# Optimization experiments

Measured on AMD Instinct MI355X. Metric: run time of the kernel, lower is better.

The kernel has to match this reference:

```python
import jax, jax.numpy as jnp
import numpy as np

EPS = 1e-15
B, N_PER, D, K, DEG = 64, 1024, 256, 64, 16  # graphs, nodes/graph, feat dim, pools/graph, avg degree


def setup_inputs() -> dict:
    key = jax.random.key(0)
    k1, k2, k3, k4 = jax.random.split(key, 4)
    N = B * N_PER
    E = B * N_PER * DEG
    x = jax.random.normal(k1, (N, D), jnp.float32)
    # edges confined within each graph (block-diagonal batched adjacency)
    rng = np.random.default_rng(0)
    offs = np.repeat(np.arange(B, dtype=np.int64) * N_PER, N_PER * DEG)
    src = rng.integers(0, N_PER, size=E) + offs
    dst = rng.integers(0, N_PER, size=E) + offs
    edge_index = jnp.asarray(np.stack([src, dst], axis=0), dtype=jnp.int32)
    edge_weight = jax.random.uniform(k2, (E,), jnp.float32)
    batch_ptr = jnp.arange(B + 1, dtype=jnp.int32) * N_PER
    W = jax.random.normal(k3, (D, K), jnp.float32) * 0.05  # pooling_net = Linear(D, K)
    b = jnp.zeros((K,), jnp.float32)
    gumbel_noise = jax.random.gumbel(k4, (N, K), jnp.float32)
    return {"x": x, "edge_weight": edge_weight, "W": W, "b": b,
            "gumbel_noise": gumbel_noise, "edge_index": edge_index, "batch_ptr": batch_ptr}


def _stochpool(x, edge_weight, W, b, gumbel_noise, edge_index, batch_ptr):
    N, Dd = x.shape
    nb = batch_ptr.shape[0] - 1          # num graphs
    n = N // nb                          # nodes per graph (equal-sized graphs)
    E = edge_index.shape[1]
    e_per = E // nb                      # edges per graph

    # pooling net + hard gumbel softmax (straight-through, tau=1)
    logits = x @ W + b                   # (N, K)
    y_soft = jax.nn.softmax(logits + gumbel_noise, axis=-1)
    y_hard = jax.nn.one_hot(jnp.argmax(y_soft, axis=-1), W.shape[1], dtype=y_soft.dtype)
    s = jax.lax.stop_gradient(y_hard - y_soft) + y_soft   # (N, K)

    u, v = edge_index[0], edge_index[1]
    graph_of_edge = u // n               # (E,) graph id per edge

    s_b = s.reshape(nb, n, -1)           # (B, n, K)
    x_b = x.reshape(nb, n, Dd)

    # pooled features: s^T x per graph
    out = jnp.einsum('bnk,bnd->bkd', s_b, x_b).reshape(nb * s_b.shape[2], Dd)

    # pooled adjacency: s^T A s per graph, via As = scatter-add over edges
    As = jnp.zeros_like(s).at[u].add(edge_weight[:, None] * s[v])   # (N, K) : (A s)
    out_adj = jnp.einsum('bnk,bnl->bkl', s_b, As.reshape(nb, n, -1))  # (B, K, K)

    # link loss: ||A - S S^T||_F per graph, via Frobenius expansion (no n x n dense)
    sq_A = jax.ops.segment_sum(edge_weight * edge_weight, graph_of_edge, num_segments=nb)
    cross = jax.ops.segment_sum(edge_weight * jnp.sum(s[u] * s[v], axis=-1),
                                graph_of_edge, num_segments=nb)
    StS = jnp.einsum('bnk,bnl->bkl', s_b, s_b)                # (B, K, K)
    sq_SSt = jnp.sum(StS * StS, axis=(1, 2))                  # ||S S^T||_F^2 = ||S^T S||_F^2
    link = jnp.sqrt(jnp.maximum(sq_A - 2.0 * cross + sq_SSt, 0.0))
    link = link / e_per                                       # normalize=True
    link_loss = jnp.mean(link)

    entropy_loss = jnp.mean(jnp.sum(-s * jnp.log(s + EPS), axis=-1))

    Kp = s_b.shape[2]
    batch = jnp.repeat(jnp.arange(nb, dtype=jnp.int32), Kp)
    batch_ptr_out = jnp.arange(0, (nb + 1) * Kp, Kp, dtype=jnp.int32)
    return out, out_adj, link_loss, entropy_loss, batch, batch_ptr_out


def reference(x, edge_weight, W, b, gumbel_noise, edge_index, batch_ptr):
    return _stochpool(x, edge_weight, W, b, gumbel_noise, edge_index, batch_ptr)
```

## Files before the change

kernel.cpp:

```cpp
#include <hip/hip_runtime.h>

#define NN 65536
#define DD 256
#define KK 64
#define NPG 1024

#define OUT_OFF   0
#define ADJ_OFF   1048576
#define LINK_OFF  1310720
#define ENT_OFF   1310721
#define BATCH_OFF 1310722
#define BPTR_OFF  1314818

#define WS_S1A    0
#define WS_C      524288
#define WS_SQP    540672
#define WS_CRP    541696
#define WS_ENTP   542720
#define WS_SORTP  552960
#define WS_GOFF   1077248
#define WS_ADJP   1093888
#define WS_NEED   (WS_ADJP + 256 * 4096 * 4)

typedef __bf16 bf16x8 __attribute__((ext_vector_type(8)));
typedef unsigned short u16x8 __attribute__((ext_vector_type(8)));
typedef float f32x4 __attribute__((ext_vector_type(4)));

static __device__ __forceinline__ unsigned short f2bf(float f) {
  unsigned int u = __float_as_uint(f);
  return (unsigned short)((u + 0x7fffu + ((u >> 16) & 1u)) >> 16);
}

__global__ __launch_bounds__(256, 4) void pool_assign_kernel(
    const float* __restrict__ x, const float* __restrict__ Wm,
    const float* __restrict__ bvec, const float* __restrict__ gum,
    int2* __restrict__ s1a, float* __restrict__ entp)
{
  __shared__ unsigned short lds_wt[64 * 264];
  __shared__ float esum[4];
  const int t    = threadIdx.x;
  const int lane = t & 63;
  const int wv   = t >> 6;
  const int q    = lane >> 4;
  const int c    = lane & 15;
  const int nb0  = blockIdx.x << 6;

  #pragma unroll 8
  for (int i = 0; i < 64; ++i) {
    int idx = (i << 8) + t;
    lds_wt[(idx & 63) * 264 + (idx >> 6)] = f2bf(Wm[idx]);
  }

  const int arow = nb0 + (wv << 4) + c;
  const float* xrow = x + (size_t)arow * DD + (q << 3);
  u16x8 afr[8];
  #pragma unroll
  for (int kb = 0; kb < 8; ++kb) {
    float4 u0 = *(const float4*)(xrow + kb * 32);
    float4 u1 = *(const float4*)(xrow + kb * 32 + 4);
    u16x8 af;
    af[0] = f2bf(u0.x); af[1] = f2bf(u0.y); af[2] = f2bf(u0.z); af[3] = f2bf(u0.w);
    af[4] = f2bf(u1.x); af[5] = f2bf(u1.y); af[6] = f2bf(u1.z); af[7] = f2bf(u1.w);
    afr[kb] = af;
  }
  __syncthreads();

  f32x4 acc[4];
  #pragma unroll
  for (int n = 0; n < 4; ++n) acc[n] = (f32x4){0.f, 0.f, 0.f, 0.f};
  #pragma unroll
  for (int n = 0; n < 4; ++n) {
    #pragma unroll
    for (int kb = 0; kb < 8; ++kb) {
      u16x8 bu = *(const u16x8*)(&lds_wt[(n * 16 + c) * 264 + kb * 32 + (q << 3)]);
      acc[n] = __builtin_amdgcn_mfma_f32_16x16x32_bf16(
          __builtin_bit_cast(bf16x8, afr[kb]),
          __builtin_bit_cast(bf16x8, bu), acc[n], 0, 0, 0);
    }
  }

  float bb[4];
  #pragma unroll
  for (int n = 0; n < 4; ++n) bb[n] = bvec[n * 16 + c];
  const int nodeq = nb0 + (wv << 4) + (q << 2);
  float ent = 0.f;
  #pragma unroll
  for (int reg = 0; reg < 4; ++reg) {
    float zz[4];
    #pragma unroll
    for (int n = 0; n < 4; ++n)
      zz[n] = acc[n][reg] + bb[n] + gum[(size_t)(nodeq + reg) * KK + n * 16 + c];
    float m = zz[0]; int a = c;
    #pragma unroll
    for (int n = 1; n < 4; ++n)
      if (zz[n] > m) { m = zz[n]; a = n * 16 + c; }
    #pragma unroll
    for (int mask = 1; mask <= 8; mask <<= 1) {
      float mo = __shfl_xor(m, mask, 64);
      int   ao = __shfl_xor(a, mask, 64);
      if (mo > m || (mo == m && ao < a)) { m = mo; a = ao; }
    }
    float ls = 0.f;
    #pragma unroll
    for (int n = 0; n < 4; ++n) ls += expf(zz[n] - m);
    #pragma unroll
    for (int mask = 1; mask <= 8; mask <<= 1) ls += __shfl_xor(ls, mask, 64);
    if (c == 0) {
      int node = nodeq + reg;
      float p  = 1.0f / ls;
      float s1 = (1.0f - p) + p;
      s1a[node] = make_int2(a, __float_as_int(s1));
      ent += -s1 * logf(s1 + 1e-15f);
    }
  }
  #pragma unroll
  for (int off = 32; off; off >>= 1) ent += __shfl_down(ent, off, 64);
  if (lane == 0) esum[wv] = ent;
  __syncthreads();
  if (t == 0) entp[blockIdx.x] = esum[0] + esum[1] + esum[2] + esum[3];
}

__global__ __launch_bounds__(256) void sort_kernel(
    const int2* __restrict__ s1a, int2* __restrict__ sortedp,
    int* __restrict__ goff, float* __restrict__ c_out)
{
  __shared__ int hist[64];
  __shared__ int offs[65];
  __shared__ int cursor[64];
  __shared__ float cbin[64];
  const int t = threadIdx.x;
  const int g = blockIdx.x;
  const int n0 = g << 10;
  if (t < 64) { hist[t] = 0; cbin[t] = 0.f; }
  __syncthreads();
  int4 p01 = ((const int4*)(s1a + n0))[t * 2];
  int4 p23 = ((const int4*)(s1a + n0))[t * 2 + 1];
  atomicAdd(&hist[p01.x], 1);
  atomicAdd(&hist[p01.z], 1);
  atomicAdd(&hist[p23.x], 1);
  atomicAdd(&hist[p23.z], 1);
  float s0 = __int_as_float(p01.y), s1v = __int_as_float(p01.w);
  float s2 = __int_as_float(p23.y), s3v = __int_as_float(p23.w);
  atomicAdd(&cbin[p01.x], s0 * s0);
  atomicAdd(&cbin[p01.z], s1v * s1v);
  atomicAdd(&cbin[p23.x], s2 * s2);
  atomicAdd(&cbin[p23.z], s3v * s3v);
  __syncthreads();
  if (t == 0) {
    int s = 0;
    #pragma unroll
    for (int k = 0; k < 64; ++k) { offs[k] = s; s += hist[k]; }
    offs[64] = s;
  }
  __syncthreads();
  if (t < 64) cursor[t] = offs[t];
  if (t < 65) goff[g * 65 + t] = offs[t];
  if (t < 64) c_out[(g << 6) + t] = cbin[t];
  __syncthreads();
  int p;
  p = atomicAdd(&cursor[p01.x], 1); sortedp[n0 + p] = make_int2(n0 + t * 4 + 0, p01.y);
  p = atomicAdd(&cursor[p01.z], 1); sortedp[n0 + p] = make_int2(n0 + t * 4 + 1, p01.w);
  p = atomicAdd(&cursor[p23.x], 1); sortedp[n0 + p] = make_int2(n0 + t * 4 + 2, p23.y);
  p = atomicAdd(&cursor[p23.z], 1); sortedp[n0 + p] = make_int2(n0 + t * 4 + 3, p23.w);
}

__global__ __launch_bounds__(256, 8) void fuse_ge_kernel(
    const float* __restrict__ x, const int2* __restrict__ sortedp,
    const int* __restrict__ goff, const int* __restrict__ src,
    const int* __restrict__ dst, const float* __restrict__ ew,
    const int2* __restrict__ s1a, float* __restrict__ out_feat,
    float* __restrict__ adjp, float* __restrict__ sqP, float* __restrict__ crP)
{
  __shared__ float adj[4096];
  __shared__ float redsq[4], redcr[4];
  const int t = threadIdx.x;
  if (blockIdx.x < 256) {
    const int blk = blockIdx.x;
    #pragma unroll
    for (int i = 0; i < 16; ++i) adj[i * 256 + t] = 0.f;
    __syncthreads();
    const int e0 = blk << 12;
    float sq = 0.f, cr = 0.f;
    #pragma unroll 4
    for (int i = 0; i < 16; ++i) {
      int e = e0 + (i << 8) + t;
      int u = src[e], v = dst[e];
      float w = ew[e];
      int2 pu = s1a[u];
      int2 pv = s1a[v];
      float contrib = w * __int_as_float(pu.y) * __int_as_float(pv.y);
      atomicAdd(&adj[pu.x * 64 + pv.x], contrib);
      sq += w * w;
      if (pu.x == pv.x) cr += contrib;
    }
    #pragma unroll
    for (int off = 32; off; off >>= 1) {
      sq += __shfl_down(sq, off, 64);
      cr += __shfl_down(cr, off, 64);
    }
    if ((t & 63) == 0) { redsq[t >> 6] = sq; redcr[t >> 6] = cr; }
    __syncthreads();
    if (t == 0) {
      sqP[blk] = redsq[0] + redsq[1] + redsq[2] + redsq[3];
      crP[blk] = redcr[0] + redcr[1] + redcr[2] + redcr[3];
    }
    float* pp = adjp + (size_t)blk * 4096;
    #pragma unroll
    for (int i = 0; i < 16; ++i) pp[i * 256 + t] = adj[i * 256 + t];
  } else {
    const int bk = blockIdx.x - 256;
    const int g = bk >> 6;
    const int k = bk & 63;
    const int o0 = goff[g * 65 + k];
    const int o1 = goff[g * 65 + k + 1];
    const int2* sp = sortedp + (g << 10);
    float sum = 0.f;
    int i = o0;
    for (; i + 4 <= o1; i += 4) {
      int2 e0 = sp[i], e1 = sp[i + 1], e2 = sp[i + 2], e3 = sp[i + 3];
      float x0 = x[(size_t)e0.x * DD + t];
      float x1 = x[(size_t)e1.x * DD + t];
      float x2 = x[(size_t)e2.x * DD + t];
      float x3 = x[(size_t)e3.x * DD + t];
      sum += __int_as_float(e0.y) * x0 + __int_as_float(e1.y) * x1
           + __int_as_float(e2.y) * x2 + __int_as_float(e3.y) * x3;
    }
    for (; i < o1; ++i) {
      int2 e = sp[i];
      sum += __int_as_float(e.y) * x[(size_t)e.x * DD + t];
    }
    out_feat[((size_t)(g * 64 + k)) * DD + t] = sum;
  }
}

__global__ __launch_bounds__(1024) void combine_fin_kernel(
    const float* __restrict__ adjp, const float* __restrict__ c,
    const float* __restrict__ sqP, const float* __restrict__ crP,
    const float* __restrict__ entp, float* __restrict__ out)
{
  __shared__ float ered[16];
  const int t = threadIdx.x;
  if (blockIdx.x < 256) {
    int idx = blockIdx.x * 1024 + t;
    int g = idx >> 12;
    int cell = idx & 4095;
    const float* p = adjp + ((size_t)(g * 4)) * 4096 + cell;
    out[ADJ_OFF + idx] = p[0] + p[4096] + p[8192] + p[12288];
    return;
  }
  float ent = entp[t];
  #pragma unroll
  for (int off = 32; off; off >>= 1) ent += __shfl_down(ent, off, 64);
  if ((t & 63) == 0) ered[t >> 6] = ent;
  float link = 0.f;
  if (t < 64) {
    const float* cg = c + t * 64;
    float ssq = 0.f;
    #pragma unroll
    for (int k = 0; k < 64; ++k) ssq += cg[k] * cg[k];
    float sq = sqP[t * 4] + sqP[t * 4 + 1] + sqP[t * 4 + 2] + sqP[t * 4 + 3];
    float cr = crP[t * 4] + crP[t * 4 + 1] + crP[t * 4 + 2] + crP[t * 4 + 3];
    float val = sq - 2.0f * cr + ssq;
    link = sqrtf(fmaxf(val, 0.f)) / 16384.0f;
    #pragma unroll
    for (int off = 32; off; off >>= 1) link += __shfl_down(link, off, 64);
  }
  __syncthreads();
  if (t == 0) {
    float es = 0.f;
    #pragma unroll
    for (int i = 0; i < 16; ++i) es += ered[i];
    out[LINK_OFF] = link / 64.0f;
    out[ENT_OFF]  = es / (float)NN;
  }
  for (int r = t; r < 4096; r += 1024) out[BATCH_OFF + r] = (float)(r >> 6);
  if (t < 65) out[BPTR_OFF + t] = (float)(t << 6);
}

__global__ __launch_bounds__(256) void edge_atomic_kernel(
    const int* __restrict__ src, const int* __restrict__ dst,
    const float* __restrict__ ew, const int2* __restrict__ s1a,
    float* __restrict__ out_adj, float* __restrict__ sqP, float* __restrict__ crP)
{
  __shared__ float adj[4096];
  __shared__ float redsq[4], redcr[4];
  const int t = threadIdx.x;
  const int blk = blockIdx.x;
  const int g = blk >> 2;
  #pragma unroll
  for (int i = 0; i < 16; ++i) adj[i * 256 + t] = 0.f;
  __syncthreads();
  const int e0 = blk << 12;
  float sq = 0.f, cr = 0.f;
  #pragma unroll 4
  for (int i = 0; i < 16; ++i) {
    int e = e0 + (i << 8) + t;
    int u = src[e], v = dst[e];
    float w = ew[e];
    int2 pu = s1a[u];
    int2 pv = s1a[v];
    float contrib = w * __int_as_float(pu.y) * __int_as_float(pv.y);
    atomicAdd(&adj[pu.x * 64 + pv.x], contrib);
    sq += w * w;
    if (pu.x == pv.x) cr += contrib;
  }
  #pragma unroll
  for (int off = 32; off; off >>= 1) {
    sq += __shfl_down(sq, off, 64);
    cr += __shfl_down(cr, off, 64);
  }
  if ((t & 63) == 0) { redsq[t >> 6] = sq; redcr[t >> 6] = cr; }
  __syncthreads();
  if (t == 0) {
    sqP[blk] = redsq[0] + redsq[1] + redsq[2] + redsq[3];
    crP[blk] = redcr[0] + redcr[1] + redcr[2] + redcr[3];
  }
  float* adjg = out_adj + (size_t)g * 4096;
  #pragma unroll
  for (int i = 0; i < 16; ++i) atomicAdd(&adjg[i * 256 + t], adj[i * 256 + t]);
}

__global__ __launch_bounds__(256, 8) void gather_kernel(
    const float* __restrict__ x, const int2* __restrict__ sortedp,
    const int* __restrict__ goff, float* __restrict__ out_feat)
{
  const int t = threadIdx.x;
  const int g = blockIdx.x >> 6;
  const int k = blockIdx.x & 63;
  const int o0 = goff[g * 65 + k];
  const int o1 = goff[g * 65 + k + 1];
  const int2* sp = sortedp + (g << 10);
  float sum = 0.f;
  for (int i = o0; i < o1; ++i) {
    int2 e = sp[i];
    sum += __int_as_float(e.y) * x[(size_t)e.x * DD + t];
  }
  out_feat[((size_t)(g * 64 + k)) * DD + t] = sum;
}

__global__ __launch_bounds__(1024) void finalize_only_kernel(
    const float* __restrict__ c, const float* __restrict__ sqP,
    const float* __restrict__ crP, const float* __restrict__ entp,
    float* __restrict__ out)
{
  __shared__ float ered[16];
  const int t = threadIdx.x;
  float ent = entp[t];
  #pragma unroll
  for (int off = 32; off; off >>= 1) ent += __shfl_down(ent, off, 64);
  if ((t & 63) == 0) ered[t >> 6] = ent;
  float link = 0.f;
  if (t < 64) {
    const float* cg = c + t * 64;
    float ssq = 0.f;
    #pragma unroll
    for (int k = 0; k < 64; ++k) ssq += cg[k] * cg[k];
    float sq = sqP[t * 4] + sqP[t * 4 + 1] + sqP[t * 4 + 2] + sqP[t * 4 + 3];
    float cr = crP[t * 4] + crP[t * 4 + 1] + crP[t * 4 + 2] + crP[t * 4 + 3];
    float val = sq - 2.0f * cr + ssq;
    link = sqrtf(fmaxf(val, 0.f)) / 16384.0f;
    #pragma unroll
    for (int off = 32; off; off >>= 1) link += __shfl_down(link, off, 64);
  }
  __syncthreads();
  if (t == 0) {
    float es = 0.f;
    #pragma unroll
    for (int i = 0; i < 16; ++i) es += ered[i];
    out[LINK_OFF] = link / 64.0f;
    out[ENT_OFF]  = es / (float)NN;
  }
  for (int r = t; r < 4096; r += 1024) out[BATCH_OFF + r] = (float)(r >> 6);
  if (t < 65) out[BPTR_OFF + t] = (float)(t << 6);
}

extern "C" void kernel_launch(void* const* d_in, const int* in_sizes, int n_in,
                              void* d_out, int out_size, void* d_ws, size_t ws_size,
                              hipStream_t stream) {
  const float* x    = (const float*)d_in[0];
  const float* ew   = (const float*)d_in[1];
  const float* Wm   = (const float*)d_in[2];
  const float* bvec = (const float*)d_in[3];
  const float* gum  = (const float*)d_in[4];
  const int*   eidx = (const int*)d_in[5];
  float* out = (float*)d_out;
  char*  ws  = (char*)d_ws;

  int2*  s1a     = (int2*)(ws + WS_S1A);
  float* c       = (float*)(ws + WS_C);
  float* sqP     = (float*)(ws + WS_SQP);
  float* crP     = (float*)(ws + WS_CRP);
  float* entp    = (float*)(ws + WS_ENTP);
  int2*  sortedp = (int2*)(ws + WS_SORTP);
  int*   goff    = (int*)(ws + WS_GOFF);
  float* adjp    = (float*)(ws + WS_ADJP);

  const int E = in_sizes[1];

  pool_assign_kernel<<<1024, 256, 0, stream>>>(x, Wm, bvec, gum, s1a, entp);
  sort_kernel<<<64, 256, 0, stream>>>(s1a, sortedp, goff, c);
  if (ws_size >= (size_t)WS_NEED) {
    fuse_ge_kernel<<<4352, 256, 0, stream>>>(x, sortedp, goff, eidx, eidx + E,
                                             ew, s1a, out + OUT_OFF, adjp, sqP, crP);
    combine_fin_kernel<<<257, 1024, 0, stream>>>(adjp, c, sqP, crP, entp, out);
  } else {
    hipMemsetAsync(out + ADJ_OFF, 0, (size_t)64 * 4096 * 4, stream);
    gather_kernel<<<4096, 256, 0, stream>>>(x, sortedp, goff, out + OUT_OFF);
    edge_atomic_kernel<<<256, 256, 0, stream>>>(eidx, eidx + E, ew, s1a,
                                                out + ADJ_OFF, sqP, crP);
    finalize_only_kernel<<<1, 1024, 0, stream>>>(c, sqP, crP, entp, out);
  }
}
```

Before: 49.19 us.

## Regroup kernels: fuse sort with edge scatter, fuse gather with combine/finalize

The per-graph sort work is merged into the edge-scatter kernel as extra blocks, since both depend only on the pool assignments. The feature gather is merged with the adjacency combine and loss finalize into one launch, because those only need sorted data and partial sums. This cuts the launch chain from four kernels to three and lets the sort run alongside the edge atomics. The cost is that the gather can no longer overlap with the edge scatter, and the finalize now runs on a 256-thread block.

Result: slower. 50.70 us (+3.1%).

```diff
diff --git a/kernel.cpp b/kernel.cpp
--- a/kernel.cpp
+++ b/kernel.cpp
@@ -120,59 +120,18 @@
   if (t == 0) entp[blockIdx.x] = esum[0] + esum[1] + esum[2] + esum[3];
 }
 
-__global__ __launch_bounds__(256) void sort_kernel(
-    const int2* __restrict__ s1a, int2* __restrict__ sortedp,
-    int* __restrict__ goff, float* __restrict__ c_out)
-{
+__global__ __launch_bounds__(256, 8) void sortedge_kernel(
+    const int* __restrict__ src, const int* __restrict__ dst,
+    const float* __restrict__ ew, const int2* __restrict__ s1a,
+    float* __restrict__ adjp, float* __restrict__ sqP, float* __restrict__ crP,
+    int2* __restrict__ sortedp, int* __restrict__ goff, float* __restrict__ c_out)
+{
+  __shared__ float adj[4096];
+  __shared__ float redsq[4], redcr[4];
   __shared__ int hist[64];
   __shared__ int offs[65];
   __shared__ int cursor[64];
   __shared__ float cbin[64];
-  const int t = threadIdx.x;
-  const int g = blockIdx.x;
-  const int n0 = g << 10;
-  if (t < 64) { hist[t] = 0; cbin[t] = 0.f; }
-  __syncthreads();
-  int4 p01 = ((const int4*)(s1a + n0))[t * 2];
-  int4 p23 = ((const int4*)(s1a + n0))[t * 2 + 1];
-  atomicAdd(&hist[p01.x], 1);
-  atomicAdd(&hist[p01.z], 1);
-  atomicAdd(&hist[p23.x], 1);
-  atomicAdd(&hist[p23.z], 1);
-  float s0 = __int_as_float(p01.y), s1v = __int_as_float(p01.w);
-  float s2 = __int_as_float(p23.y), s3v = __int_as_float(p23.w);
-  atomicAdd(&cbin[p01.x], s0 * s0);
-  atomicAdd(&cbin[p01.z], s1v * s1v);
-  atomicAdd(&cbin[p23.x], s2 * s2);
-  atomicAdd(&cbin[p23.z], s3v * s3v);
-  __syncthreads();
-  if (t == 0) {
-    int s = 0;
-    #pragma unroll
-    for (int k = 0; k < 64; ++k) { offs[k] = s; s += hist[k]; }
-    offs[64] = s;
-  }
-  __syncthreads();
-  if (t < 64) cursor[t] = offs[t];
-  if (t < 65) goff[g * 65 + t] = offs[t];
-  if (t < 64) c_out[(g << 6) + t] = cbin[t];
-  __syncthreads();
-  int p;
-  p = atomicAdd(&cursor[p01.x], 1); sortedp[n0 + p] = make_int2(n0 + t * 4 + 0, p01.y);
-  p = atomicAdd(&cursor[p01.z], 1); sortedp[n0 + p] = make_int2(n0 + t * 4 + 1, p01.w);
-  p = atomicAdd(&cursor[p23.x], 1); sortedp[n0 + p] = make_int2(n0 + t * 4 + 2, p23.y);
-  p = atomicAdd(&cursor[p23.z], 1); sortedp[n0 + p] = make_int2(n0 + t * 4 + 3, p23.w);
-}
-
-__global__ __launch_bounds__(256, 8) void fuse_ge_kernel(
-    const float* __restrict__ x, const int2* __restrict__ sortedp,
-    const int* __restrict__ goff, const int* __restrict__ src,
-    const int* __restrict__ dst, const float* __restrict__ ew,
-    const int2* __restrict__ s1a, float* __restrict__ out_feat,
-    float* __restrict__ adjp, float* __restrict__ sqP, float* __restrict__ crP)
-{
-  __shared__ float adj[4096];
-  __shared__ float redsq[4], redcr[4];
   const int t = threadIdx.x;
   if (blockIdx.x < 256) {
     const int blk = blockIdx.x;
@@ -208,9 +167,54 @@
     #pragma unroll
     for (int i = 0; i < 16; ++i) pp[i * 256 + t] = adj[i * 256 + t];
   } else {
-    const int bk = blockIdx.x - 256;
-    const int g = bk >> 6;
-    const int k = bk & 63;
+    const int g = blockIdx.x - 256;
+    const int n0 = g << 10;
+    if (t < 64) { hist[t] = 0; cbin[t] = 0.f; }
+    __syncthreads();
+    int4 p01 = ((const int4*)(s1a + n0))[t * 2];
+    int4 p23 = ((const int4*)(s1a + n0))[t * 2 + 1];
+    atomicAdd(&hist[p01.x], 1);
+    atomicAdd(&hist[p01.z], 1);
+    atomicAdd(&hist[p23.x], 1);
+    atomicAdd(&hist[p23.z], 1);
+    float s0 = __int_as_float(p01.y), s1v = __int_as_float(p01.w);
+    float s2 = __int_as_float(p23.y), s3v = __int_as_float(p23.w);
+    atomicAdd(&cbin[p01.x], s0 * s0);
+    atomicAdd(&cbin[p01.z], s1v * s1v);
+    atomicAdd(&cbin[p23.x], s2 * s2);
+    atomicAdd(&cbin[p23.z], s3v * s3v);
+    __syncthreads();
+    if (t == 0) {
+      int s = 0;
+      #pragma unroll
+      for (int k = 0; k < 64; ++k) { offs[k] = s; s += hist[k]; }
+      offs[64] = s;
+    }
+    __syncthreads();
+    if (t < 64) cursor[t] = offs[t];
+    if (t < 65) goff[g * 65 + t] = offs[t];
+    if (t < 64) c_out[(g << 6) + t] = cbin[t];
+    __syncthreads();
+    int p;
+    p = atomicAdd(&cursor[p01.x], 1); sortedp[n0 + p] = make_int2(n0 + t * 4 + 0, p01.y);
+    p = atomicAdd(&cursor[p01.z], 1); sortedp[n0 + p] = make_int2(n0 + t * 4 + 1, p01.w);
+    p = atomicAdd(&cursor[p23.x], 1); sortedp[n0 + p] = make_int2(n0 + t * 4 + 2, p23.y);
+    p = atomicAdd(&cursor[p23.z], 1); sortedp[n0 + p] = make_int2(n0 + t * 4 + 3, p23.w);
+  }
+}
+
+__global__ __launch_bounds__(256, 8) void gatherfin_kernel(
+    const float* __restrict__ x, const int2* __restrict__ sortedp,
+    const int* __restrict__ goff, const float* __restrict__ adjp,
+    const float* __restrict__ c, const float* __restrict__ sqP,
+    const float* __restrict__ crP, const float* __restrict__ entp,
+    float* __restrict__ out)
+{
+  __shared__ float ered[4];
+  const int t = threadIdx.x;
+  if (blockIdx.x < 4096) {
+    const int g = blockIdx.x >> 6;
+    const int k = blockIdx.x & 63;
     const int o0 = goff[g * 65 + k];
     const int o1 = goff[g * 65 + k + 1];
     const int2* sp = sortedp + (g << 10);
@@ -229,52 +233,43 @@
       int2 e = sp[i];
       sum += __int_as_float(e.y) * x[(size_t)e.x * DD + t];
     }
-    out_feat[((size_t)(g * 64 + k)) * DD + t] = sum;
-  }
-}
-
-__global__ __launch_bounds__(1024) void combine_fin_kernel(
-    const float* __restrict__ adjp, const float* __restrict__ c,
-    const float* __restrict__ sqP, const float* __restrict__ crP,
-    const float* __restrict__ entp, float* __restrict__ out)
-{
-  __shared__ float ered[16];
-  const int t = threadIdx.x;
-  if (blockIdx.x < 256) {
-    int idx = blockIdx.x * 1024 + t;
-    int g = idx >> 12;
-    int cell = idx & 4095;
-    const float* p = adjp + ((size_t)(g * 4)) * 4096 + cell;
-    out[ADJ_OFF + idx] = p[0] + p[4096] + p[8192] + p[12288];
-    return;
-  }
-  float ent = entp[t];
-  #pragma unroll
-  for (int off = 32; off; off >>= 1) ent += __shfl_down(ent, off, 64);
-  if ((t & 63) == 0) ered[t >> 6] = ent;
-  float link = 0.f;
-  if (t < 64) {
-    const float* cg = c + t * 64;
-    float ssq = 0.f;
-    #pragma unroll
-    for (int k = 0; k < 64; ++k) ssq += cg[k] * cg[k];
-    float sq = sqP[t * 4] + sqP[t * 4 + 1] + sqP[t * 4 + 2] + sqP[t * 4 + 3];
-    float cr = crP[t * 4] + crP[t * 4 + 1] + crP[t * 4 + 2] + crP[t * 4 + 3];
-    float val = sq - 2.0f * cr + ssq;
-    link = sqrtf(fmaxf(val, 0.f)) / 16384.0f;
-    #pragma unroll
-    for (int off = 32; off; off >>= 1) link += __shfl_down(link, off, 64);
-  }
-  __syncthreads();
-  if (t == 0) {
-    float es = 0.f;
-    #pragma unroll
-    for (int i = 0; i < 16; ++i) es += ered[i];
-    out[LINK_OFF] = link / 64.0f;
-    out[ENT_OFF]  = es / (float)NN;
-  }
-  for (int r = t; r < 4096; r += 1024) out[BATCH_OFF + r] = (float)(r >> 6);
-  if (t < 65) out[BPTR_OFF + t] = (float)(t << 6);
+    out[OUT_OFF + ((size_t)((g << 6) + k)) * DD + t] = sum;
+  } else if (blockIdx.x < 4352) {
+    const int blkc = blockIdx.x - 4096;
+    #pragma unroll
+    for (int i = 0; i < 4; ++i) {
+      int idx = blkc * 1024 + (i << 8) + t;
+      int g = idx >> 12;
+      int cell = idx & 4095;
+      const float* p = adjp + ((size_t)(g * 4)) * 4096 + cell;
+      out[ADJ_OFF + idx] = p[0] + p[4096] + p[8192] + p[12288];
+    }
+  } else {
+    float ent = entp[t] + entp[t + 256] + entp[t + 512] + entp[t + 768];
+    #pragma unroll
+    for (int off = 32; off; off >>= 1) ent += __shfl_down(ent, off, 64);
+    if ((t & 63) == 0) ered[t >> 6] = ent;
+    float link = 0.f;
+    if (t < 64) {
+      const float* cg = c + t * 64;
+      float ssq = 0.f;
+      #pragma unroll
+      for (int k = 0; k < 64; ++k) ssq += cg[k] * cg[k];
+      float sq = sqP[t * 4] + sqP[t * 4 + 1] + sqP[t * 4 + 2] + sqP[t * 4 + 3];
+      float cr = crP[t * 4] + crP[t * 4 + 1] + crP[t * 4 + 2] + crP[t * 4 + 3];
+      float val = sq - 2.0f * cr + ssq;
+      link = sqrtf(fmaxf(val, 0.f)) / 16384.0f;
+      #pragma unroll
+      for (int off = 32; off; off >>= 1) link += __shfl_down(link, off, 64);
+    }
+    __syncthreads();
+    if (t == 0) {
+      out[LINK_OFF] = link / 64.0f;
+      out[ENT_OFF]  = (ered[0] + ered[1] + ered[2] + ered[3]) / (float)NN;
+    }
+    for (int r = t; r < 4096; r += 256) out[BATCH_OFF + r] = (float)(r >> 6);
+    for (int i = t; i < 65; i += 256)   out[BPTR_OFF + i]  = (float)(i << 6);
+  }
 }
 
 __global__ __launch_bounds__(256) void edge_atomic_kernel(
@@ -320,6 +315,50 @@
   for (int i = 0; i < 16; ++i) atomicAdd(&adjg[i * 256 + t], adj[i * 256 + t]);
 }
 
+__global__ __launch_bounds__(256) void sort_only_kernel(
+    const int2* __restrict__ s1a, int2* __restrict__ sortedp,
+    int* __restrict__ goff, float* __restrict__ c_out)
+{
+  __shared__ int hist[64];
+  __shared__ int offs[65];
+  __shared__ int cursor[64];
+  __shared__ float cbin[64];
+  const int t = threadIdx.x;
+  const int g = blockIdx.x;
+  const int n0 = g << 10;
+  if (t < 64) { hist[t] = 0; cbin[t] = 0.f; }
+  __syncthreads();
+  int4 p01 = ((const int4*)(s1a + n0))[t * 2];
+  int4 p23 = ((const int4*)(s1a + n0))[t * 2 + 1];
+  atomicAdd(&hist[p01.x], 1);
+  atomicAdd(&hist[p01.z], 1);
+  atomicAdd(&hist[p23.x], 1);
+  atomicAdd(&hist[p23.z], 1);
+  float s0 = __int_as_float(p01.y), s1v = __int_as_float(p01.w);
+  float s2 = __int_as_float(p23.y), s3v = __int_as_float(p23.w);
+  atomicAdd(&cbin[p01.x], s0 * s0);
+  atomicAdd(&cbin[p01.z], s1v * s1v);
+  atomicAdd(&cbin[p23.x], s2 * s2);
+  atomicAdd(&cbin[p23.z], s3v * s3v);
+  __syncthreads();
+  if (t == 0) {
+    int s = 0;
+    #pragma unroll
+    for (int k = 0; k < 64; ++k) { offs[k] = s; s += hist[k]; }
+    offs[64] = s;
+  }
+  __syncthreads();
+  if (t < 64) cursor[t] = offs[t];
+  if (t < 65) goff[g * 65 + t] = offs[t];
+  if (t < 64) c_out[(g << 6) + t] = cbin[t];
+  __syncthreads();
+  int p;
+  p = atomicAdd(&cursor[p01.x], 1); sortedp[n0 + p] = make_int2(n0 + t * 4 + 0, p01.y);
+  p = atomicAdd(&cursor[p01.z], 1); sortedp[n0 + p] = make_int2(n0 + t * 4 + 1, p01.w);
+  p = atomicAdd(&cursor[p23.x], 1); sortedp[n0 + p] = make_int2(n0 + t * 4 + 2, p23.y);
+  p = atomicAdd(&cursor[p23.z], 1); sortedp[n0 + p] = make_int2(n0 + t * 4 + 3, p23.w);
+}
+
 __global__ __launch_bounds__(256, 8) void gather_kernel(
     const float* __restrict__ x, const int2* __restrict__ sortedp,
     const int* __restrict__ goff, float* __restrict__ out_feat)
@@ -335,17 +374,17 @@
     int2 e = sp[i];
     sum += __int_as_float(e.y) * x[(size_t)e.x * DD + t];
   }
-  out_feat[((size_t)(g * 64 + k)) * DD + t] = sum;
-}
-
-__global__ __launch_bounds__(1024) void finalize_only_kernel(
+  out_feat[((size_t)((g << 6) + k)) * DD + t] = sum;
+}
+
+__global__ __launch_bounds__(256) void finalize_only_kernel(
     const float* __restrict__ c, const float* __restrict__ sqP,
     const float* __restrict__ crP, const float* __restrict__ entp,
     float* __restrict__ out)
 {
-  __shared__ float ered[16];
-  const int t = threadIdx.x;
-  float ent = entp[t];
+  __shared__ float ered[4];
+  const int t = threadIdx.x;
+  float ent = entp[t] + entp[t + 256] + entp[t + 512] + entp[t + 768];
   #pragma unroll
   for (int off = 32; off; off >>= 1) ent += __shfl_down(ent, off, 64);
   if ((t & 63) == 0) ered[t >> 6] = ent;
@@ -364,14 +403,11 @@
   }
   __syncthreads();
   if (t == 0) {
-    float es = 0.f;
-    #pragma unroll
-    for (int i = 0; i < 16; ++i) es += ered[i];
     out[LINK_OFF] = link / 64.0f;
-    out[ENT_OFF]  = es / (float)NN;
-  }
-  for (int r = t; r < 4096; r += 1024) out[BATCH_OFF + r] = (float)(r >> 6);
-  if (t < 65) out[BPTR_OFF + t] = (float)(t << 6);
+    out[ENT_OFF]  = (ered[0] + ered[1] + ered[2] + ered[3]) / (float)NN;
+  }
+  for (int r = t; r < 4096; r += 256) out[BATCH_OFF + r] = (float)(r >> 6);
+  for (int i = t; i < 65; i += 256)   out[BPTR_OFF + i]  = (float)(i << 6);
 }
 
 extern "C" void kernel_launch(void* const* d_in, const int* in_sizes, int n_in,
@@ -398,16 +434,17 @@
   const int E = in_sizes[1];
 
   pool_assign_kernel<<<1024, 256, 0, stream>>>(x, Wm, bvec, gum, s1a, entp);
-  sort_kernel<<<64, 256, 0, stream>>>(s1a, sortedp, goff, c);
   if (ws_size >= (size_t)WS_NEED) {
-    fuse_ge_kernel<<<4352, 256, 0, stream>>>(x, sortedp, goff, eidx, eidx + E,
-                                             ew, s1a, out + OUT_OFF, adjp, sqP, crP);
-    combine_fin_kernel<<<257, 1024, 0, stream>>>(adjp, c, sqP, crP, entp, out);
+    sortedge_kernel<<<320, 256, 0, stream>>>(eidx, eidx + E, ew, s1a,
+                                             adjp, sqP, crP, sortedp, goff, c);
+    gatherfin_kernel<<<4353, 256, 0, stream>>>(x, sortedp, goff, adjp,
+                                               c, sqP, crP, entp, out);
   } else {
     hipMemsetAsync(out + ADJ_OFF, 0, (size_t)64 * 4096 * 4, stream);
+    sort_only_kernel<<<64, 256, 0, stream>>>(s1a, sortedp, goff, c);
     gather_kernel<<<4096, 256, 0, stream>>>(x, sortedp, goff, out + OUT_OFF);
     edge_atomic_kernel<<<256, 256, 0, stream>>>(eidx, eidx + E, ew, s1a,
                                                 out + ADJ_OFF, sqP, crP);
-    finalize_only_kernel<<<1, 1024, 0, stream>>>(c, sqP, crP, entp, out);
-  }
-}
+    finalize_only_kernel<<<1, 256, 0, stream>>>(c, sqP, crP, entp, out);
+  }
+}
```
